# Performance work log

Hardware: AMD Instinct MI355X
Metric: run time of the kernel (lower is better)

## Reference

```python
import jax, jax.numpy as jnp
import numpy as np

M = 150        # AR2 tail-fit window
LAM = 1e-3     # ridge regularizer in the 2x2 solve
CLIP_K = 4.0   # soft clip multiplier
H = 96         # forecast horizon (base_model.H)


def setup_inputs() -> dict:
    key = jax.random.key(0)
    k1, k2 = jax.random.split(key)
    x = jax.random.normal(k1, (32, 512, 2048), dtype=jnp.float32)
    W = jax.random.normal(k2, (2048, 96), dtype=jnp.float32) * 0.02
    return {"x": x, "W": W}


def _ar2_forecast(x):
    # x: (B, C, L); closed-form AR2 fit on last M samples, vectorized over (B, C)
    y = x[..., -M:]                     # (B, C, M)
    Y = y[..., 2:]                      # targets
    p1 = y[..., 1:-1]
    p2 = y[..., :-2]
    s = lambda a, b: jnp.sum(a * b, axis=-1)
    A11 = s(p1, p1) + LAM
    A22 = s(p2, p2) + LAM
    A12 = s(p1, p2)
    b1 = s(p1, Y)
    b2 = s(p2, Y)
    det = A11 * A22 - A12 * A12
    a1 = (b1 * A22 - b2 * A12) / det    # (B, C)
    a2 = (A11 * b2 - A12 * b1) / det

    def step(carry, _):
        y1, y2 = carry
        yn = a1 * y1 + a2 * y2
        return (yn, y1), yn

    _, out = jax.lax.scan(step, (x[..., -1], x[..., -2]), None, length=H)
    return jnp.moveaxis(out, 0, -1)     # (B, C, H)


def reference(x, W):
    # AR2 part is computed on detached history in the original (numpy round-trip)
    Yb = jax.lax.stop_gradient(_ar2_forecast(x))
    d_hat = jnp.einsum('bcl,lh->bch', x, W)          # base model: per-channel linear head
    y_hat = Yb + d_hat
    last = x[..., -1:]                               # (B, C, 1), broadcasts over H
    hstd = jnp.maximum(jnp.std(x, axis=-1, ddof=1, keepdims=True), 1e-6)  # torch unbiased std
    return jnp.clip(y_hat, last - CLIP_K * hstd, last + CLIP_K * hstd)
```

## Files before the change

### kernel.cpp

```cpp
#include <hip/hip_runtime.h>
#include <math.h>

constexpr int L     = 2048;
constexpr int NH    = 96;
constexpr int MLEN  = 150;
constexpr int NAR   = 148;
constexpr float LAM    = 0.001f;
constexpr float CLIP_K = 4.0f;

typedef __attribute__((ext_vector_type(8))) short short8;
typedef __attribute__((ext_vector_type(4))) float floatx4;

__device__ inline short f2bf(float f) {
    union { float f; unsigned u; } v; v.f = f;
    unsigned r = v.u + 0x7FFFu + ((v.u >> 16) & 1u);
    return (short)(r >> 16);
}

__global__ __launch_bounds__(256) void wt_kernel(
    const float* __restrict__ W, short* __restrict__ Wt)
{
    int idx = blockIdx.x * 256 + threadIdx.x;
    int n = idx >> 11;
    int k = idx & 2047;
    Wt[idx] = f2bf(W[k * NH + n]);
}

__global__ __launch_bounds__(64) void gemm_ar2_kernel(
    const float* __restrict__ x, const short* __restrict__ Wt,
    float* __restrict__ out)
{
    __shared__ float Ys[16][NH + 1];

    const int lane = threadIdx.x;
    const int m    = lane & 15;
    const int quad = lane >> 4;
    const int row0 = blockIdx.x * 16;

    const float* arow  = x  + (size_t)(row0 + m) * L + quad * 8;
    const short* wbase = Wt + (size_t)m * L + quad * 8;

    floatx4 acc[6];
    #pragma unroll
    for (int j = 0; j < 6; ++j) acc[j] = floatx4{0.f, 0.f, 0.f, 0.f};

    float sum = 0.f, sumsq = 0.f;

    float4 a0_c = *(const float4*)(arow + 0);
    float4 a1_c = *(const float4*)(arow + 4);
    float4 a0_n = *(const float4*)(arow + 32);
    float4 a1_n = *(const float4*)(arow + 36);
    short8 b_c[6];
    #pragma unroll
    for (int j = 0; j < 6; ++j) b_c[j] = *(const short8*)(wbase + j * 16 * L);

    for (int step = 0; step < 64; ++step) {
        int k2 = (step + 2 < 64) ? (step + 2) * 32 : step * 32;
        int k1 = (step + 1 < 64) ? (step + 1) * 32 : step * 32;
        float4 a0_p = *(const float4*)(arow + k2);
        float4 a1_p = *(const float4*)(arow + k2 + 4);
        short8 b_n[6];
        #pragma unroll
        for (int j = 0; j < 6; ++j)
            b_n[j] = *(const short8*)(wbase + j * 16 * L + k1);

        sum   += ((a0_c.x + a0_c.y) + (a0_c.z + a0_c.w))
               + ((a1_c.x + a1_c.y) + (a1_c.z + a1_c.w));
        sumsq = fmaf(a0_c.x, a0_c.x, sumsq); sumsq = fmaf(a0_c.y, a0_c.y, sumsq);
        sumsq = fmaf(a0_c.z, a0_c.z, sumsq); sumsq = fmaf(a0_c.w, a0_c.w, sumsq);
        sumsq = fmaf(a1_c.x, a1_c.x, sumsq); sumsq = fmaf(a1_c.y, a1_c.y, sumsq);
        sumsq = fmaf(a1_c.z, a1_c.z, sumsq); sumsq = fmaf(a1_c.w, a1_c.w, sumsq);

        short8 af;
        af[0] = f2bf(a0_c.x); af[1] = f2bf(a0_c.y);
        af[2] = f2bf(a0_c.z); af[3] = f2bf(a0_c.w);
        af[4] = f2bf(a1_c.x); af[5] = f2bf(a1_c.y);
        af[6] = f2bf(a1_c.z); af[7] = f2bf(a1_c.w);

        #pragma unroll
        for (int j = 0; j < 6; ++j)
            acc[j] = __builtin_amdgcn_mfma_f32_16x16x32_bf16(af, b_c[j], acc[j], 0, 0, 0);

        a0_c = a0_n; a1_c = a1_n;
        a0_n = a0_p; a1_n = a1_p;
        #pragma unroll
        for (int j = 0; j < 6; ++j) b_c[j] = b_n[j];
    }

    sum   += __shfl_xor(sum,   16); sum   += __shfl_xor(sum,   32);
    sumsq += __shfl_xor(sumsq, 16); sumsq += __shfl_xor(sumsq, 32);

    const float* ytail = x + (size_t)(row0 + m) * L + (L - MLEN);
    float A11 = 0.f, A22 = 0.f, A12 = 0.f, b1 = 0.f, b2 = 0.f;
    for (int i = quad; i < NAR; i += 4) {
        float p2v = ytail[i];
        float p1v = ytail[i + 1];
        float Yv  = ytail[i + 2];
        A11 = fmaf(p1v, p1v, A11);
        A22 = fmaf(p2v, p2v, A22);
        A12 = fmaf(p1v, p2v, A12);
        b1  = fmaf(p1v, Yv,  b1);
        b2  = fmaf(p2v, Yv,  b2);
    }
    A11 += __shfl_xor(A11, 16); A11 += __shfl_xor(A11, 32);
    A22 += __shfl_xor(A22, 16); A22 += __shfl_xor(A22, 32);
    A12 += __shfl_xor(A12, 16); A12 += __shfl_xor(A12, 32);
    b1  += __shfl_xor(b1,  16); b1  += __shfl_xor(b1,  32);
    b2  += __shfl_xor(b2,  16); b2  += __shfl_xor(b2,  32);

    float lo = 0.f, hi = 0.f;
    if (quad == 0) {
        A11 += LAM; A22 += LAM;
        float det = A11 * A22 - A12 * A12;
        float a1c = (b1 * A22 - b2 * A12) / det;
        float a2c = (A11 * b2 - A12 * b1) / det;

        float last = ytail[MLEN - 1];
        float y1 = last;
        float y2 = ytail[MLEN - 2];
        for (int n = 0; n < NH; ++n) {
            float yn = a1c * y1 + a2c * y2;
            Ys[m][n] = yn;
            y2 = y1; y1 = yn;
        }
        float var  = (sumsq - sum * sum * (1.0f / L)) * (1.0f / (L - 1));
        float hstd = fmaxf(sqrtf(fmaxf(var, 0.f)), 1e-6f);
        lo = last - CLIP_K * hstd;
        hi = last + CLIP_K * hstd;
    }
    __syncthreads();

    #pragma unroll
    for (int reg = 0; reg < 4; ++reg) {
        int r = quad * 4 + reg;
        float rlo = __shfl(lo, r);
        float rhi = __shfl(hi, r);
        #pragma unroll
        for (int j = 0; j < 6; ++j) {
            int c = 16 * j + m;
            float v = acc[j][reg] + Ys[r][c];
            v = fminf(fmaxf(v, rlo), rhi);
            out[(size_t)(row0 + r) * NH + c] = v;
        }
    }
}

extern "C" void kernel_launch(void* const* d_in, const int* in_sizes, int n_in,
                              void* d_out, int out_size, void* d_ws, size_t ws_size,
                              hipStream_t stream) {
    const float* x = (const float*)d_in[0];
    const float* W = (const float*)d_in[1];
    float* out = (float*)d_out;
    short* Wt  = (short*)d_ws;

    wt_kernel<<<dim3((NH * L) / 256), dim3(256), 0, stream>>>(W, Wt);

    const int rows = 32 * 512;
    gemm_ar2_kernel<<<dim3(rows / 16), dim3(64), 0, stream>>>(x, Wt, out);
}
```

Measured before the change: 228.9 us.

## Split GEMM K dimension across four waves with LDS partial-sum reduction

Each 16-row block now uses four waves, and each wave handles a quarter of the 2048-long K loop. Waves 1-3 write their MFMA partial accumulators and their sum/sumsq partials to LDS, and wave 0 reduces them and runs the AR2 fit and the clipped store. This shortens the per-block serial K loop and puts more waves in flight to hide memory latency on a bandwidth-bound workload. The cost is extra LDS traffic, a block barrier, three idle waves during the epilogue, and a single-wave s_waitcnt standing in for the later barrier.

```diff
diff --git a/kernel.cpp b/kernel.cpp
--- a/kernel.cpp
+++ b/kernel.cpp
@@ -7,6 +7,10 @@
 constexpr int NAR   = 148;
 constexpr float LAM    = 0.001f;
 constexpr float CLIP_K = 4.0f;
+
+constexpr int NWAVE = 4;
+constexpr int KPW   = L / NWAVE;
+constexpr int STEPS = KPW / 32;
 
 typedef __attribute__((ext_vector_type(8))) short short8;
 typedef __attribute__((ext_vector_type(4))) float floatx4;
@@ -26,19 +30,23 @@
     Wt[idx] = f2bf(W[k * NH + n]);
 }
 
-__global__ __launch_bounds__(64) void gemm_ar2_kernel(
+__global__ __launch_bounds__(256, 4) void gemm_ar2_kernel(
     const float* __restrict__ x, const short* __restrict__ Wt,
     float* __restrict__ out)
 {
+    __shared__ float accP[NWAVE - 1][64][24];
+    __shared__ float sumP[NWAVE][16], sumsqP[NWAVE][16];
     __shared__ float Ys[16][NH + 1];
 
-    const int lane = threadIdx.x;
+    const int t    = threadIdx.x;
+    const int lane = t & 63;
+    const int wv   = t >> 6;
     const int m    = lane & 15;
     const int quad = lane >> 4;
     const int row0 = blockIdx.x * 16;
 
-    const float* arow  = x  + (size_t)(row0 + m) * L + quad * 8;
-    const short* wbase = Wt + (size_t)m * L + quad * 8;
+    const float* arow  = x  + (size_t)(row0 + m) * L + wv * KPW + quad * 8;
+    const short* wbase = Wt + (size_t)m * L        + wv * KPW + quad * 8;
 
     floatx4 acc[6];
     #pragma unroll
@@ -54,9 +62,9 @@
     #pragma unroll
     for (int j = 0; j < 6; ++j) b_c[j] = *(const short8*)(wbase + j * 16 * L);
 
-    for (int step = 0; step < 64; ++step) {
-        int k2 = (step + 2 < 64) ? (step + 2) * 32 : step * 32;
-        int k1 = (step + 1 < 64) ? (step + 1) * 32 : step * 32;
+    for (int step = 0; step < STEPS; ++step) {
+        int k2 = (step + 2 < STEPS) ? (step + 2) * 32 : step * 32;
+        int k1 = (step + 1 < STEPS) ? (step + 1) * 32 : step * 32;
         float4 a0_p = *(const float4*)(arow + k2);
         float4 a1_p = *(const float4*)(arow + k2 + 4);
         short8 b_n[6];
@@ -89,6 +97,29 @@
 
     sum   += __shfl_xor(sum,   16); sum   += __shfl_xor(sum,   32);
     sumsq += __shfl_xor(sumsq, 16); sumsq += __shfl_xor(sumsq, 32);
+    if (quad == 0) { sumP[wv][m] = sum; sumsqP[wv][m] = sumsq; }
+
+    if (wv > 0) {
+        #pragma unroll
+        for (int j = 0; j < 6; ++j)
+            #pragma unroll
+            for (int r = 0; r < 4; ++r)
+                accP[wv - 1][lane][j * 4 + r] = acc[j][r];
+    }
+    __syncthreads();
+
+    if (wv != 0) return;
+
+    #pragma unroll
+    for (int w = 0; w < NWAVE - 1; ++w)
+        #pragma unroll
+        for (int j = 0; j < 6; ++j)
+            #pragma unroll
+            for (int r = 0; r < 4; ++r)
+                acc[j][r] += accP[w][lane][j * 4 + r];
+
+    float sumT   = sumP[0][m]   + sumP[1][m]   + sumP[2][m]   + sumP[3][m];
+    float sumsqT = sumsqP[0][m] + sumsqP[1][m] + sumsqP[2][m] + sumsqP[3][m];
 
     const float* ytail = x + (size_t)(row0 + m) * L + (L - MLEN);
     float A11 = 0.f, A22 = 0.f, A12 = 0.f, b1 = 0.f, b2 = 0.f;
@@ -123,12 +154,12 @@
             Ys[m][n] = yn;
             y2 = y1; y1 = yn;
         }
-        float var  = (sumsq - sum * sum * (1.0f / L)) * (1.0f / (L - 1));
+        float var  = (sumsqT - sumT * sumT * (1.0f / L)) * (1.0f / (L - 1));
         float hstd = fmaxf(sqrtf(fmaxf(var, 0.f)), 1e-6f);
         lo = last - CLIP_K * hstd;
         hi = last + CLIP_K * hstd;
     }
-    __syncthreads();
+    asm volatile("s_waitcnt lgkmcnt(0)" ::: "memory");
 
     #pragma unroll
     for (int reg = 0; reg < 4; ++reg) {
@@ -156,5 +187,5 @@
     wt_kernel<<<dim3((NH * L) / 256), dim3(256), 0, stream>>>(W, Wt);
 
     const int rows = 32 * 512;
-    gemm_ar2_kernel<<<dim3(rows / 16), dim3(64), 0, stream>>>(x, Wt, out);
+    gemm_ar2_kernel<<<dim3(rows / 16), dim3(256), 0, stream>>>(x, Wt, out);
 }
```

After: 233.1 us. Within noise of the previous version (+1.8%).

## Stage x tiles through LDS with async global_load_lds and split N across waves

Applied to the files above, without the earlier changes.

Each block now handles 32 rows with 4 waves. Each wave takes 16 rows and half of the 96 output columns. The x tile is streamed into XOR-swizzled, double-buffered shared memory using the direct global-to-LDS load builtin, so every A element is read from global memory once and shared by two waves. This replaces the per-lane register prefetch of x. The change adds a block barrier on every K step and cuts MFMA work per wave in half. That may hurt latency hiding, and W fragments are still loaded per wave.

```diff
diff --git a/kernel.cpp b/kernel.cpp
--- a/kernel.cpp
+++ b/kernel.cpp
@@ -7,6 +7,9 @@
 constexpr int NAR   = 148;
 constexpr float LAM    = 0.001f;
 constexpr float CLIP_K = 4.0f;
+
+constexpr int TM    = 32;
+constexpr int STEPS = L / 32;
 
 typedef __attribute__((ext_vector_type(8))) short short8;
 typedef __attribute__((ext_vector_type(4))) float floatx4;
@@ -26,121 +29,142 @@
     Wt[idx] = f2bf(W[k * NH + n]);
 }
 
-__global__ __launch_bounds__(64) void gemm_ar2_kernel(
+__global__ __launch_bounds__(256) void gemm_ar2_kernel(
     const float* __restrict__ x, const short* __restrict__ Wt,
     float* __restrict__ out)
 {
-    __shared__ float Ys[16][NH + 1];
+    __shared__ float As[2][TM * 32];
+    __shared__ float Ys[TM][NH + 1];
+    __shared__ float los[TM], his[TM];
 
-    const int lane = threadIdx.x;
+    const int t    = threadIdx.x;
+    const int lane = t & 63;
+    const int wv   = t >> 6;
+    const int h    = wv >> 1;
+    const int g    = wv & 1;
     const int m    = lane & 15;
     const int quad = lane >> 4;
-    const int row0 = blockIdx.x * 16;
+    const int row0 = blockIdx.x * TM;
+    const int r    = h * 16 + m;
 
-    const float* arow  = x  + (size_t)(row0 + m) * L + quad * 8;
-    const short* wbase = Wt + (size_t)m * L + quad * 8;
+    const int sr = wv * 8 + (lane >> 3);
+    const int sc = lane & 7;
+    const int gc = sc ^ (sr & 7);
+    const float* sgptr = x + (size_t)(row0 + sr) * L + gc * 4;
 
-    floatx4 acc[6];
+    const short* wbase = Wt + (size_t)(48 * g + m) * L + quad * 8;
+
+    floatx4 acc[3];
     #pragma unroll
-    for (int j = 0; j < 6; ++j) acc[j] = floatx4{0.f, 0.f, 0.f, 0.f};
+    for (int jj = 0; jj < 3; ++jj) acc[jj] = floatx4{0.f, 0.f, 0.f, 0.f};
 
     float sum = 0.f, sumsq = 0.f;
 
-    float4 a0_c = *(const float4*)(arow + 0);
-    float4 a1_c = *(const float4*)(arow + 4);
-    float4 a0_n = *(const float4*)(arow + 32);
-    float4 a1_n = *(const float4*)(arow + 36);
-    short8 b_c[6];
+    __builtin_amdgcn_global_load_lds(
+        (const __attribute__((address_space(1))) unsigned int*)sgptr,
+        (__attribute__((address_space(3))) unsigned int*)&As[0][wv * 256],
+        16, 0, 0);
+    short8 b_c[3], b_n[3];
     #pragma unroll
-    for (int j = 0; j < 6; ++j) b_c[j] = *(const short8*)(wbase + j * 16 * L);
+    for (int jj = 0; jj < 3; ++jj)
+        b_c[jj] = *(const short8*)(wbase + jj * 16 * L);
 
-    for (int step = 0; step < 64; ++step) {
-        int k2 = (step + 2 < 64) ? (step + 2) * 32 : step * 32;
-        int k1 = (step + 1 < 64) ? (step + 1) * 32 : step * 32;
-        float4 a0_p = *(const float4*)(arow + k2);
-        float4 a1_p = *(const float4*)(arow + k2 + 4);
-        short8 b_n[6];
+    const int p0 = (2 * quad)     ^ (r & 7);
+    const int p1 = (2 * quad + 1) ^ (r & 7);
+
+    for (int s = 0; s < STEPS; ++s) {
+        const int cur = s & 1;
+        __syncthreads();
+
+        if (s + 1 < STEPS)
+            __builtin_amdgcn_global_load_lds(
+                (const __attribute__((address_space(1))) unsigned int*)(sgptr + (s + 1) * 32),
+                (__attribute__((address_space(3))) unsigned int*)&As[cur ^ 1][wv * 256],
+                16, 0, 0);
+
+        const int k1 = (s + 1 < STEPS) ? (s + 1) * 32 : s * 32;
         #pragma unroll
-        for (int j = 0; j < 6; ++j)
-            b_n[j] = *(const short8*)(wbase + j * 16 * L + k1);
+        for (int jj = 0; jj < 3; ++jj)
+            b_n[jj] = *(const short8*)(wbase + jj * 16 * L + k1);
 
-        sum   += ((a0_c.x + a0_c.y) + (a0_c.z + a0_c.w))
-               + ((a1_c.x + a1_c.y) + (a1_c.z + a1_c.w));
-        sumsq = fmaf(a0_c.x, a0_c.x, sumsq); sumsq = fmaf(a0_c.y, a0_c.y, sumsq);
-        sumsq = fmaf(a0_c.z, a0_c.z, sumsq); sumsq = fmaf(a0_c.w, a0_c.w, sumsq);
-        sumsq = fmaf(a1_c.x, a1_c.x, sumsq); sumsq = fmaf(a1_c.y, a1_c.y, sumsq);
-        sumsq = fmaf(a1_c.z, a1_c.z, sumsq); sumsq = fmaf(a1_c.w, a1_c.w, sumsq);
+        float4 f0 = *(const float4*)(&As[cur][r * 32 + p0 * 4]);
+        float4 f1 = *(const float4*)(&As[cur][r * 32 + p1 * 4]);
+
+        if (g == 0) {
+            sum  += ((f0.x + f0.y) + (f0.z + f0.w))
+                  + ((f1.x + f1.y) + (f1.z + f1.w));
+            sumsq = fmaf(f0.x, f0.x, sumsq); sumsq = fmaf(f0.y, f0.y, sumsq);
+            sumsq = fmaf(f0.z, f0.z, sumsq); sumsq = fmaf(f0.w, f0.w, sumsq);
+            sumsq = fmaf(f1.x, f1.x, sumsq); sumsq = fmaf(f1.y, f1.y, sumsq);
+            sumsq = fmaf(f1.z, f1.z, sumsq); sumsq = fmaf(f1.w, f1.w, sumsq);
+        }
 
         short8 af;
-        af[0] = f2bf(a0_c.x); af[1] = f2bf(a0_c.y);
-        af[2] = f2bf(a0_c.z); af[3] = f2bf(a0_c.w);
-        af[4] = f2bf(a1_c.x); af[5] = f2bf(a1_c.y);
-        af[6] = f2bf(a1_c.z); af[7] = f2bf(a1_c.w);
+        af[0] = f2bf(f0.x); af[1] = f2bf(f0.y); af[2] = f2bf(f0.z); af[3] = f2bf(f0.w);
+        af[4] = f2bf(f1.x); af[5] = f2bf(f1.y); af[6] = f2bf(f1.z); af[7] = f2bf(f1.w);
 
         #pragma unroll
-        for (int j = 0; j < 6; ++j)
-            acc[j] = __builtin_amdgcn_mfma_f32_16x16x32_bf16(af, b_c[j], acc[j], 0, 0, 0);
+        for (int jj = 0; jj < 3; ++jj)
+            acc[jj] = __builtin_amdgcn_mfma_f32_16x16x32_bf16(af, b_c[jj], acc[jj], 0, 0, 0);
 
-        a0_c = a0_n; a1_c = a1_n;
-        a0_n = a0_p; a1_n = a1_p;
         #pragma unroll
-        for (int j = 0; j < 6; ++j) b_c[j] = b_n[j];
+        for (int jj = 0; jj < 3; ++jj) b_c[jj] = b_n[jj];
     }
 
-    sum   += __shfl_xor(sum,   16); sum   += __shfl_xor(sum,   32);
-    sumsq += __shfl_xor(sumsq, 16); sumsq += __shfl_xor(sumsq, 32);
+    if (g == 0) {
+        sum   += __shfl_xor(sum,   16); sum   += __shfl_xor(sum,   32);
+        sumsq += __shfl_xor(sumsq, 16); sumsq += __shfl_xor(sumsq, 32);
 
-    const float* ytail = x + (size_t)(row0 + m) * L + (L - MLEN);
-    float A11 = 0.f, A22 = 0.f, A12 = 0.f, b1 = 0.f, b2 = 0.f;
-    for (int i = quad; i < NAR; i += 4) {
-        float p2v = ytail[i];
-        float p1v = ytail[i + 1];
-        float Yv  = ytail[i + 2];
-        A11 = fmaf(p1v, p1v, A11);
-        A22 = fmaf(p2v, p2v, A22);
-        A12 = fmaf(p1v, p2v, A12);
-        b1  = fmaf(p1v, Yv,  b1);
-        b2  = fmaf(p2v, Yv,  b2);
-    }
-    A11 += __shfl_xor(A11, 16); A11 += __shfl_xor(A11, 32);
-    A22 += __shfl_xor(A22, 16); A22 += __shfl_xor(A22, 32);
-    A12 += __shfl_xor(A12, 16); A12 += __shfl_xor(A12, 32);
-    b1  += __shfl_xor(b1,  16); b1  += __shfl_xor(b1,  32);
-    b2  += __shfl_xor(b2,  16); b2  += __shfl_xor(b2,  32);
+        const float* ytail = x + (size_t)(row0 + r) * L + (L - MLEN);
+        float A11 = 0.f, A22 = 0.f, A12 = 0.f, b1 = 0.f, b2 = 0.f;
+        for (int i = quad; i < NAR; i += 4) {
+            float p2v = ytail[i];
+            float p1v = ytail[i + 1];
+            float Yv  = ytail[i + 2];
+            A11 = fmaf(p1v, p1v, A11);
+            A22 = fmaf(p2v, p2v, A22);
+            A12 = fmaf(p1v, p2v, A12);
+            b1  = fmaf(p1v, Yv,  b1);
+            b2  = fmaf(p2v, Yv,  b2);
+        }
+        A11 += __shfl_xor(A11, 16); A11 += __shfl_xor(A11, 32);
+        A22 += __shfl_xor(A22, 16); A22 += __shfl_xor(A22, 32);
+        A12 += __shfl_xor(A12, 16); A12 += __shfl_xor(A12, 32);
+        b1  += __shfl_xor(b1,  16); b1  += __shfl_xor(b1,  32);
+        b2  += __shfl_xor(b2,  16); b2  += __shfl_xor(b2,  32);
 
-    float lo = 0.f, hi = 0.f;
-    if (quad == 0) {
-        A11 += LAM; A22 += LAM;
-        float det = A11 * A22 - A12 * A12;
-        float a1c = (b1 * A22 - b2 * A12) / det;
-        float a2c = (A11 * b2 - A12 * b1) / det;
+        if (quad == 0) {
+            A11 += LAM; A22 += LAM;
+            float det = A11 * A22 - A12 * A12;
+            float a1c = (b1 * A22 - b2 * A12) / det;
+            float a2c = (A11 * b2 - A12 * b1) / det;
 
-        float last = ytail[MLEN - 1];
-        float y1 = last;
-        float y2 = ytail[MLEN - 2];
-        for (int n = 0; n < NH; ++n) {
-            float yn = a1c * y1 + a2c * y2;
-            Ys[m][n] = yn;
-            y2 = y1; y1 = yn;
+            float last = ytail[MLEN - 1];
+            float y1 = last;
+            float y2 = ytail[MLEN - 2];
+            for (int n = 0; n < NH; ++n) {
+                float yn = a1c * y1 + a2c * y2;
+                Ys[r][n] = yn;
+                y2 = y1; y1 = yn;
+            }
+            float var  = (sumsq - sum * sum * (1.0f / L)) * (1.0f / (L - 1));
+            float hstd = fmaxf(sqrtf(fmaxf(var, 0.f)), 1e-6f);
+            los[r] = last - CLIP_K * hstd;
+            his[r] = last + CLIP_K * hstd;
         }
-        float var  = (sumsq - sum * sum * (1.0f / L)) * (1.0f / (L - 1));
-        float hstd = fmaxf(sqrtf(fmaxf(var, 0.f)), 1e-6f);
-        lo = last - CLIP_K * hstd;
-        hi = last + CLIP_K * hstd;
     }
     __syncthreads();
 
     #pragma unroll
     for (int reg = 0; reg < 4; ++reg) {
-        int r = quad * 4 + reg;
-        float rlo = __shfl(lo, r);
-        float rhi = __shfl(hi, r);
+        int rl = h * 16 + quad * 4 + reg;
+        float lo = los[rl], hi = his[rl];
         #pragma unroll
-        for (int j = 0; j < 6; ++j) {
-            int c = 16 * j + m;
-            float v = acc[j][reg] + Ys[r][c];
-            v = fminf(fmaxf(v, rlo), rhi);
-            out[(size_t)(row0 + r) * NH + c] = v;
+        for (int jj = 0; jj < 3; ++jj) {
+            int c = (3 * g + jj) * 16 + m;
+            float v = acc[jj][reg] + Ys[rl][c];
+            v = fminf(fmaxf(v, lo), hi);
+            out[(size_t)(row0 + rl) * NH + c] = v;
         }
     }
 }
@@ -156,5 +180,5 @@
     wt_kernel<<<dim3((NH * L) / 256), dim3(256), 0, stream>>>(W, Wt);
 
     const int rows = 32 * 512;
-    gemm_ar2_kernel<<<dim3(rows / 16), dim3(64), 0, stream>>>(x, Wt, out);
+    gemm_ar2_kernel<<<dim3(rows / TM), dim3(256), 0, stream>>>(x, Wt, out);
 }
```

Result: slower. 234.9 us (+2.6%).
